# Kernel tuning notes

Hardware: AMD Instinct MI355X
Metric: run time of the kernel (lower is better)

Reference implementation:

```python
import jax, jax.numpy as jnp
import numpy as np

N, E, HID, H, L, EF = 50000, 640000, 128, 8, 3, 16
C = HID // H  # 16, per-head output channels (concat=True)
NEG_SLOPE = 0.2
LN_EPS = 1e-5


def setup_inputs() -> dict:
    key = jax.random.key(0)
    ks = jax.random.split(key, 12)
    s = 0.05
    x = jax.random.normal(ks[0], (N, HID), jnp.float32)
    batch_index = jnp.sort(jax.random.randint(ks[1], (N,), 0, 64, dtype=jnp.int32))
    edge_index = jax.random.randint(ks[2], (2, E), 0, N, dtype=jnp.int32)
    edge_attr = jax.random.normal(ks[3], (E, EF), jnp.float32)
    # edge_transform: Linear(EF, HID)
    Wt = jax.random.normal(ks[4], (EF, HID), jnp.float32) * s
    bt = jnp.zeros((HID,), jnp.float32)
    # per-layer GATv2 params (stacked over L layers)
    Wl = jax.random.normal(ks[5], (L, HID, HID), jnp.float32) * s  # lin_l (source)
    bl = jnp.zeros((L, HID), jnp.float32)
    Wr = jax.random.normal(ks[6], (L, HID, HID), jnp.float32) * s  # lin_r (target)
    br = jnp.zeros((L, HID), jnp.float32)
    We = jax.random.normal(ks[7], (L, HID, HID), jnp.float32) * s  # lin_edge (no bias)
    att = jax.random.normal(ks[8], (L, H, C), jnp.float32) * s
    bias_o = jnp.zeros((L, HID), jnp.float32)
    ln_g = jnp.ones((L, HID), jnp.float32)
    ln_b = jnp.zeros((L, HID), jnp.float32)
    return dict(x=x, batch_index=batch_index, edge_index=edge_index, edge_attr=edge_attr,
                Wt=Wt, bt=bt, Wl=Wl, bl=bl, Wr=Wr, br=br, We=We, att=att,
                bias_o=bias_o, ln_g=ln_g, ln_b=ln_b)


def _layer_norm(x, g, b):
    mu = jnp.mean(x, axis=-1, keepdims=True)
    var = jnp.var(x, axis=-1, keepdims=True)
    return g * (x - mu) * jax.lax.rsqrt(var + LN_EPS) + b


def _gatv2_layer(x, ea, src, dst, Wl, bl, Wr, br, We, att, bias_o):
    # node transforms: lin_l for source features, lin_r for target features
    xl = (x @ Wl + bl).reshape(N, H, C)
    xr = (x @ Wr + br).reshape(N, H, C)
    em = (ea @ We).reshape(E, H, C)
    # per-edge attention logits (GATv2: leaky_relu AFTER the sum, then dot with att)
    m = jax.nn.leaky_relu(xl[src] + xr[dst] + em, NEG_SLOPE)  # [E,H,C]
    logits = jnp.einsum('ehc,hc->eh', m, att)                  # [E,H]
    # segment softmax over incoming edges of each destination node
    lmax = jax.ops.segment_max(logits, dst, num_segments=N)    # [N,H]
    p = jnp.exp(logits - lmax[dst])
    denom = jax.ops.segment_sum(p, dst, num_segments=N)        # [N,H]
    alpha = p / (denom[dst] + 1e-16)
    # weighted scatter-aggregate of source messages
    out = jax.ops.segment_sum(xl[src] * alpha[:, :, None], dst, num_segments=N)  # [N,H,C]
    return out.reshape(N, HID) + bias_o


def reference(x, batch_index, edge_index, edge_attr, Wt, bt, Wl, bl, Wr, br, We, att, bias_o, ln_g, ln_b):
    src, dst = edge_index[0], edge_index[1]
    ea = edge_attr @ Wt + bt  # shared edge_transform, [E,HID]
    for l in range(L):
        out = _gatv2_layer(x, ea, src, dst, Wl[l], bl[l], Wr[l], br[l], We[l], att[l], bias_o[l])
        out = _layer_norm(out, ln_g[l], ln_b[l])
        x = jax.nn.relu(out) + x  # dropout p=0 -> identity; residual
    return x
```

## Files before the change

kernel.cpp:

```cpp
#include <hip/hip_runtime.h>

#define N_NODES 50000
#define N_EDGES 640000
#define HID 128
#define EF 16
#define NLAYERS 3
#define CHUNK 16
#define SCAN_BLOCKS 196

typedef __attribute__((ext_vector_type(8))) short short8;
typedef __attribute__((ext_vector_type(8))) _Float16 half8;
typedef __attribute__((ext_vector_type(4))) float f32x4;
typedef __attribute__((ext_vector_type(2))) float f32x2;

__device__ __forceinline__ unsigned short f2bf(float f) {
  unsigned int u = __float_as_uint(f);
  u = u + 0x7FFFu + ((u >> 16) & 1u);
  return (unsigned short)(u >> 16);
}

__device__ __forceinline__ unsigned short f2h(float f) {
  _Float16 h = (_Float16)f;
  return *(unsigned short*)&h;
}

__device__ __forceinline__ float dpp_hadd8(float v) {
  int x;
  x = __builtin_amdgcn_update_dpp(0, __float_as_int(v), 0xB1, 0xF, 0xF, true);
  v += __int_as_float(x);
  x = __builtin_amdgcn_update_dpp(0, __float_as_int(v), 0x4E, 0xF, 0xF, true);
  v += __int_as_float(x);
  x = __builtin_amdgcn_update_dpp(0, __float_as_int(v), 0x141, 0xF, 0xF, true);
  v += __int_as_float(x);
  return v;
}

__device__ __forceinline__ f32x2 pk_add(f32x2 a, f32x2 b) {
  f32x2 d;
  asm("v_pk_add_f32 %0, %1, %2" : "=v"(d) : "v"(a), "v"(b));
  return d;
}
__device__ __forceinline__ f32x2 pk_mul(f32x2 a, f32x2 b) {
  f32x2 d;
  asm("v_pk_mul_f32 %0, %1, %2" : "=v"(d) : "v"(a), "v"(b));
  return d;
}

__device__ __forceinline__ int pslot(int j) {
  return (((j >> 4) * 8 + (j & 7)) << 1) + ((j >> 3) & 1);
}

__global__ __launch_bounds__(256) void k_setup(const float* __restrict__ Wt,
                                               const float* __restrict__ bt,
                                               const float* __restrict__ We,
                                               const float* __restrict__ Wl,
                                               const float* __restrict__ Wr,
                                               const float* __restrict__ x,
                                               float* __restrict__ ct,
                                               unsigned short* __restrict__ MtB,
                                               unsigned short* __restrict__ WT,
                                               unsigned short* __restrict__ xbf) {
  int b = blockIdx.x, t = threadIdx.x;
  if (b < 26) {
    int id = b * 256 + t;
    const int total = NLAYERS * (EF + 1) * HID;
    if (id >= total) return;
    int l = id / ((EF + 1) * HID);
    int r = id % ((EF + 1) * HID);
    int row = r / HID;
    int j = r % HID;
    const float* Wel = We + l * HID * HID;
    float s = 0.f;
    if (row < EF) {
      const float* wtr = Wt + row * HID;
      for (int i = 0; i < HID; ++i) s += wtr[i] * Wel[i * HID + j];
      int blk = j >> 4, nn = j & 15;
      size_t base = (size_t)(l * 8 + blk) * 64;
      MtB[(base + (size_t)((row >> 3) * 16 + nn)) * 8 + (row & 7)] = f2h(s);
      MtB[(base + (size_t)((2 + (row >> 3)) * 16 + nn)) * 8 + (row & 7)] = 0;
    } else {
      for (int i = 0; i < HID; ++i) s += bt[i] * Wel[i * HID + j];
      ct[l * HID + pslot(j)] = s;
    }
  } else if (b < 410) {
    int id = (b - 26) * 256 + t;
    int k = id & (HID - 1);
    int n = (id >> 7) & (HID - 1);
    int s = (id >> 14) & 1;
    int l = id >> 15;
    const float* W = (s == 0 ? Wl : Wr) + (size_t)l * HID * HID;
    WT[id] = f2bf(W[k * HID + n]);
  } else {
    int id = (b - 410) * 256 + t;
    const float4* p = (const float4*)(x + (size_t)id * 8);
    float4 a = p[0], bb = p[1];
    unsigned short o[8] = {f2bf(a.x), f2bf(a.y), f2bf(a.z), f2bf(a.w),
                           f2bf(bb.x), f2bf(bb.y), f2bf(bb.z), f2bf(bb.w)};
    *(uint4*)(xbf + (size_t)id * 8) = *(uint4*)o;
  }
}

__global__ __launch_bounds__(256) void k_hist(const int* __restrict__ dst, int* __restrict__ counts) {
  int e = blockIdx.x * 256 + threadIdx.x;
  if (e < N_EDGES) atomicAdd(&counts[dst[e]], 1);
}

__global__ __launch_bounds__(256) void k_scan1(const int* __restrict__ counts,
                                               int* __restrict__ rowptr,
                                               int* __restrict__ bsum) {
  __shared__ int sc[256];
  int t = threadIdx.x;
  int i = blockIdx.x * 256 + t;
  int v = (i < N_NODES) ? counts[i] : 0;
  sc[t] = v;
  __syncthreads();
  for (int off = 1; off < 256; off <<= 1) {
    int u = 0;
    if (t >= off) u = sc[t - off];
    __syncthreads();
    sc[t] += u;
    __syncthreads();
  }
  if (i < N_NODES) rowptr[i] = sc[t] - v;
  if (t == 255) bsum[blockIdx.x] = sc[255];
}

__global__ __launch_bounds__(256) void k_scan2(int* __restrict__ bsum) {
  __shared__ int sc[256];
  int t = threadIdx.x;
  int v = (t < SCAN_BLOCKS) ? bsum[t] : 0;
  sc[t] = v;
  __syncthreads();
  for (int off = 1; off < 256; off <<= 1) {
    int u = 0;
    if (t >= off) u = sc[t - off];
    __syncthreads();
    sc[t] += u;
    __syncthreads();
  }
  bsum[t] = sc[t] - v;
}

__global__ __launch_bounds__(256) void k_scan3(int* __restrict__ rowptr, const int* __restrict__ bsum) {
  int t = threadIdx.x;
  int i = blockIdx.x * 256 + t;
  if (i < N_NODES) rowptr[i] += bsum[blockIdx.x];
  if (i == 0) rowptr[N_NODES] = N_EDGES;
}

__global__ __launch_bounds__(256) void k_fill(const int* __restrict__ src,
                                              const int* __restrict__ dst,
                                              const int* __restrict__ rowptr,
                                              int* __restrict__ fill,
                                              int* __restrict__ ssrc,
                                              const float* __restrict__ eattr,
                                              unsigned short* __restrict__ eaA) {
  int e = blockIdx.x * 256 + threadIdx.x;
  if (e >= N_EDGES) return;
  int d = dst[e];
  int pos = atomicAdd(&fill[d], 1);
  int idx = rowptr[d] + pos;
  ssrc[idx] = src[e] << 6;
  const float* pe = eattr + (size_t)e * EF;
  unsigned short* po = eaA + (size_t)idx * 32;
#pragma unroll
  for (int g = 0; g < 2; ++g) {
    unsigned short o[8];
#pragma unroll
    for (int k = 0; k < 8; ++k) o[k] = f2h(pe[g * 8 + k]);
    *(uint4*)(po + g * 8) = *(uint4*)o;
  }
  uint4 z = {0u, 0u, 0u, 0u};
  *(uint4*)(po + 16) = z;
  *(uint4*)(po + 24) = z;
}

__global__ __launch_bounds__(256) void k_gemm_mfma(const unsigned short* __restrict__ xbf,
                                                   const unsigned short* __restrict__ WTl,
                                                   const float* __restrict__ bl,
                                                   const float* __restrict__ br,
                                                   const float* __restrict__ ctl,
                                                   unsigned short* __restrict__ xlb,
                                                   unsigned short* __restrict__ xrb) {
  __shared__ short As[64 * 136];
  __shared__ short Bs[128 * 136];
  int t = threadIdx.x;
  int s = blockIdx.y;
  int row0 = blockIdx.x * 64;

  const uint4* gx = (const uint4*)xbf;
#pragma unroll
  for (int p = 0; p < 4; ++p) {
    int c = t + p * 256;
    int row = c >> 4, col16 = c & 15;
    int grow = row0 + row;
    if (grow >= N_NODES) grow = N_NODES - 1;
    uint4 v = gx[grow * 16 + col16];
    *(uint4*)(&As[row * 136 + col16 * 8]) = v;
  }
  const uint4* gw = (const uint4*)WTl;
#pragma unroll
  for (int p = 0; p < 8; ++p) {
    int c = t + p * 256;
    int row = c >> 4, col16 = c & 15;
    uint4 v = gw[s * 2048 + row * 16 + col16];
    *(uint4*)(&Bs[row * 136 + col16 * 8]) = v;
  }
  __syncthreads();

  int lane = t & 63, w = t >> 6;
  int quad = lane >> 4, lm = lane & 15;
  f32x4 acc[4][2];
#pragma unroll
  for (int mf = 0; mf < 4; ++mf)
#pragma unroll
    for (int nf = 0; nf < 2; ++nf) acc[mf][nf] = (f32x4)(0.f);

#pragma unroll
  for (int ks = 0; ks < 4; ++ks) {
    short8 af[4], bf[2];
#pragma unroll
    for (int mf = 0; mf < 4; ++mf)
      af[mf] = *(short8*)(&As[(mf * 16 + lm) * 136 + ks * 32 + quad * 8]);
#pragma unroll
    for (int nf = 0; nf < 2; ++nf)
      bf[nf] = *(short8*)(&Bs[(w * 32 + nf * 16 + lm) * 136 + ks * 32 + quad * 8]);
#pragma unroll
    for (int mf = 0; mf < 4; ++mf)
#pragma unroll
      for (int nf = 0; nf < 2; ++nf)
        acc[mf][nf] = __builtin_amdgcn_mfma_f32_16x16x32_bf16(af[mf], bf[nf], acc[mf][nf], 0, 0, 0);
  }

  const float* bias = (s == 0) ? bl : br;
  unsigned short* out = (s == 0) ? xlb : xrb;
#pragma unroll
  for (int nf = 0; nf < 2; ++nf) {
    int n = w * 32 + nf * 16 + lm;
    int slot = pslot(n);
    float bv = bias[n] + ((s == 1) ? ctl[slot] : 0.f);
#pragma unroll
    for (int mf = 0; mf < 4; ++mf) {
#pragma unroll
      for (int r = 0; r < 4; ++r) {
        int grow = row0 + mf * 16 + quad * 4 + r;
        if (grow < N_NODES) out[(size_t)grow * HID + slot] = f2bf(acc[mf][nf][r] + bv);
      }
    }
  }
}

__global__ __launch_bounds__(64) void k_fused(const float* __restrict__ xin,
                                              const unsigned int* __restrict__ xlb,
                                              const unsigned int* __restrict__ xrb,
                                              const int* __restrict__ rowptr,
                                              const int* __restrict__ ssrc,
                                              const unsigned short* __restrict__ eaA,
                                              const unsigned int* __restrict__ MtBl,
                                              const float* __restrict__ att,
                                              const float* __restrict__ bias_o,
                                              const float* __restrict__ lng,
                                              const float* __restrict__ lnb,
                                              float* __restrict__ xout,
                                              unsigned short* __restrict__ xbf_out) {
  __shared__ __align__(16) float em_s[CHUNK * 130];
  __shared__ int src_s[CHUNK + 8];
  int n = blockIdx.x;
  int l = threadIdx.x;
  int lm = l & 15, quad = l >> 4;
  int j0 = (l >> 3) * 16 + (l & 7), j1 = j0 + 8;

  uint4 bfr[8];
  const uint4* mb = (const uint4*)MtBl;
#pragma unroll
  for (int b = 0; b < 8; ++b) bfr[b] = mb[b * 64 + l];

  unsigned int ur = xrb[(size_t)n * 64 + l];
  f32x2 base;
  base.x = __uint_as_float(ur << 16);
  base.y = __uint_as_float(ur & 0xFFFF0000u);
  const float LOG2E = 1.44269504088896340736f;
  f32x2 attp = {att[j0] * LOG2E, att[j1] * LOG2E};
  f32x2 c02 = {0.2f, 0.2f};
  int beg = rowptr[n], end = rowptr[n + 1];

  f32x2 acc = {0.f, 0.f};
  float denom = 0.f;

  for (int c0 = beg; c0 < end; c0 += CHUNK) {
    int cnt = min(CHUNK, end - c0);
    if (l < cnt) src_s[l] = ssrc[c0 + l];
    if (l < 8) src_s[cnt + l] = 0;

    half8 af = *(const half8*)(eaA + (size_t)(c0 + lm) * 32 + quad * 8);
    f32x4 cc[8];
#pragma unroll
    for (int b = 0; b < 8; ++b)
      cc[b] = __builtin_amdgcn_mfma_f32_16x16x32_f16(af, *(half8*)&bfr[b], (f32x4)(0.f), 0, 0, 0);
#pragma unroll
    for (int b = 0; b < 8; ++b)
#pragma unroll
      for (int r = 0; r < 4; ++r)
        em_s[(quad * 4 + r) * 130 + ((b * 8 + (lm & 7)) << 1) + (lm >> 3)] = cc[b][r];

    auto edge = [&](int i, unsigned int u) {
      f32x2 xls;
      xls.x = __uint_as_float(u << 16);
      xls.y = __uint_as_float(u & 0xFFFF0000u);
      f32x2 em = *(const f32x2*)(&em_s[i * 130 + 2 * l]);
      f32x2 m = pk_add(pk_add(base, xls), em);
      f32x2 ms = pk_mul(c02, m);
      m.x = fmaxf(m.x, ms.x);
      m.y = fmaxf(m.y, ms.y);
      f32x2 v2 = pk_mul(m, attp);
      float vs = dpp_hadd8(v2.x + v2.y);
      float p = exp2f(vs);
      denom += p;
      acc.x = fmaf(xls.x, p, acc.x);
      acc.y = fmaf(xls.y, p, acc.y);
    };

    unsigned int cur[4];
#pragma unroll
    for (int q = 0; q < 4; ++q) cur[q] = xlb[src_s[q] + l];
    int cnt4 = cnt & ~3;
    for (int i = 0; i < cnt4; i += 4) {
      unsigned int nxt[4];
#pragma unroll
      for (int q = 0; q < 4; ++q) nxt[q] = xlb[src_s[i + 4 + q] + l];
#pragma unroll
      for (int q = 0; q < 4; ++q) edge(i + q, cur[q]);
#pragma unroll
      for (int q = 0; q < 4; ++q) cur[q] = nxt[q];
    }
#pragma unroll
    for (int q = 0; q < 4; ++q)
      if (cnt4 + q < cnt) edge(cnt4 + q, cur[q]);
  }

  f32x2 outp;
  float inv = 1.f / (denom + 1e-16f);
  outp.x = acc.x * inv + bias_o[j0];
  outp.y = acc.y * inv + bias_o[j1];
  float s1 = outp.x + outp.y;
  float s2 = outp.x * outp.x + outp.y * outp.y;
#pragma unroll
  for (int mask = 1; mask <= 32; mask <<= 1) {
    s1 += __shfl_xor(s1, mask);
    s2 += __shfl_xor(s2, mask);
  }
  float mu = s1 * (1.f / 128.f);
  float var = s2 * (1.f / 128.f) - mu * mu;
  float rs = rsqrtf(var + 1e-5f);
  float y0 = lng[j0] * (outp.x - mu) * rs + lnb[j0];
  float y1 = lng[j1] * (outp.y - mu) * rs + lnb[j1];
  float r0 = fmaxf(y0, 0.f) + xin[(size_t)n * HID + j0];
  float r1 = fmaxf(y1, 0.f) + xin[(size_t)n * HID + j1];
  xout[(size_t)n * HID + j0] = r0;
  xout[(size_t)n * HID + j1] = r1;
  xbf_out[(size_t)n * HID + j0] = f2bf(r0);
  xbf_out[(size_t)n * HID + j1] = f2bf(r1);
}

extern "C" void kernel_launch(void* const* d_in, const int* in_sizes, int n_in,
                              void* d_out, int out_size, void* d_ws, size_t ws_size,
                              hipStream_t stream) {
  const float* x0    = (const float*)d_in[0];
  const int*   eidx  = (const int*)d_in[2];
  const float* eattr = (const float*)d_in[3];
  const float* Wt    = (const float*)d_in[4];
  const float* bt    = (const float*)d_in[5];
  const float* Wl    = (const float*)d_in[6];
  const float* bl    = (const float*)d_in[7];
  const float* Wr    = (const float*)d_in[8];
  const float* br    = (const float*)d_in[9];
  const float* We    = (const float*)d_in[10];
  const float* att   = (const float*)d_in[11];
  const float* bo    = (const float*)d_in[12];
  const float* lng   = (const float*)d_in[13];
  const float* lnb   = (const float*)d_in[14];
  float* out = (float*)d_out;
  const int* src = eidx;
  const int* dst = eidx + N_EDGES;

  char* ws = (char*)d_ws;
  size_t off = 0;
  auto alloc = [&](size_t bytes) {
    char* p = ws + off;
    off += (bytes + 255) & ~(size_t)255;
    return p;
  };
  int* counts = (int*)alloc((size_t)N_NODES * 4);
  int* fill   = (int*)alloc((size_t)N_NODES * 4);
  float* ct   = (float*)alloc((size_t)NLAYERS * HID * 4);
  int* rowptr = (int*)alloc((size_t)(N_NODES + 1) * 4);
  int* bsum   = (int*)alloc(256 * 4);
  int* ssrc   = (int*)alloc((size_t)N_EDGES * 4);
  unsigned short* eaA = (unsigned short*)alloc(((size_t)N_EDGES + 16) * 32 * 2);
  unsigned short* MtB = (unsigned short*)alloc((size_t)NLAYERS * 8 * 64 * 8 * 2);
  unsigned short* xlb = (unsigned short*)alloc((size_t)N_NODES * HID * 2);
  unsigned short* xrb = (unsigned short*)alloc((size_t)N_NODES * HID * 2);
  float* xbuf = (float*)alloc((size_t)N_NODES * HID * 4);
  unsigned short* xbf = (unsigned short*)alloc((size_t)N_NODES * HID * 2);
  unsigned short* WTb = (unsigned short*)alloc((size_t)NLAYERS * 2 * HID * HID * 2);

  hipMemsetAsync(counts, 0, (char*)(fill + N_NODES) - (char*)counts, stream);

  hipLaunchKernelGGL(k_setup, dim3(3535), dim3(256), 0, stream,
                     Wt, bt, We, Wl, Wr, x0, ct, MtB, WTb, xbf);
  hipLaunchKernelGGL(k_hist, dim3((N_EDGES + 255) / 256), dim3(256), 0, stream, dst, counts);
  hipLaunchKernelGGL(k_scan1, dim3(SCAN_BLOCKS), dim3(256), 0, stream, counts, rowptr, bsum);
  hipLaunchKernelGGL(k_scan2, dim3(1), dim3(256), 0, stream, bsum);
  hipLaunchKernelGGL(k_scan3, dim3(SCAN_BLOCKS), dim3(256), 0, stream, rowptr, bsum);
  hipLaunchKernelGGL(k_fill, dim3((N_EDGES + 255) / 256), dim3(256), 0, stream,
                     src, dst, rowptr, fill, ssrc, eattr, eaA);

  for (int l = 0; l < NLAYERS; ++l) {
    const float* xin = (l == 0) ? x0 : (const float*)xbuf;
    float* xout = (l == NLAYERS - 1) ? out : xbuf;
    hipLaunchKernelGGL(k_gemm_mfma, dim3((N_NODES + 63) / 64, 2), dim3(256), 0, stream,
                       xbf, WTb + (size_t)l * 2 * HID * HID, bl + l * HID, br + l * HID,
                       ct + (size_t)l * HID, xlb, xrb);
    hipLaunchKernelGGL(k_fused, dim3(N_NODES), dim3(64), 0, stream,
                       xin, (const unsigned int*)xlb, (const unsigned int*)xrb,
                       rowptr, ssrc, eaA,
                       (const unsigned int*)(MtB + (size_t)l * 8 * 64 * 8),
                       att + l * HID,
                       bo + l * HID, lng + l * HID, lnb + l * HID, xout, xbf);
  }
}
```

Before: 441.3 us.

## Merge histogram into setup, store edge terms as fp16 pairs, prefetch 8 sources

Measured after the change: 505.3 us. 14.5% more time.

```diff
diff --git a/kernel.cpp b/kernel.cpp
--- a/kernel.cpp
+++ b/kernel.cpp
@@ -10,6 +10,7 @@
 
 typedef __attribute__((ext_vector_type(8))) short short8;
 typedef __attribute__((ext_vector_type(8))) _Float16 half8;
+typedef __attribute__((ext_vector_type(2))) __fp16 fp16x2;
 typedef __attribute__((ext_vector_type(4))) float f32x4;
 typedef __attribute__((ext_vector_type(2))) float f32x2;
 
@@ -56,6 +57,8 @@
                                                const float* __restrict__ Wl,
                                                const float* __restrict__ Wr,
                                                const float* __restrict__ x,
+                                               const int* __restrict__ dst,
+                                               int* __restrict__ counts,
                                                float* __restrict__ ct,
                                                unsigned short* __restrict__ MtB,
                                                unsigned short* __restrict__ WT,
@@ -90,19 +93,17 @@
     int l = id >> 15;
     const float* W = (s == 0 ? Wl : Wr) + (size_t)l * HID * HID;
     WT[id] = f2bf(W[k * HID + n]);
-  } else {
+  } else if (b < 3535) {
     int id = (b - 410) * 256 + t;
     const float4* p = (const float4*)(x + (size_t)id * 8);
     float4 a = p[0], bb = p[1];
     unsigned short o[8] = {f2bf(a.x), f2bf(a.y), f2bf(a.z), f2bf(a.w),
                            f2bf(bb.x), f2bf(bb.y), f2bf(bb.z), f2bf(bb.w)};
     *(uint4*)(xbf + (size_t)id * 8) = *(uint4*)o;
-  }
-}
-
-__global__ __launch_bounds__(256) void k_hist(const int* __restrict__ dst, int* __restrict__ counts) {
-  int e = blockIdx.x * 256 + threadIdx.x;
-  if (e < N_EDGES) atomicAdd(&counts[dst[e]], 1);
+  } else {
+    int e = (b - 3535) * 256 + t;
+    if (e < N_EDGES) atomicAdd(&counts[dst[e]], 1);
+  }
 }
 
 __global__ __launch_bounds__(256) void k_scan1(const int* __restrict__ counts,
@@ -263,7 +264,7 @@
                                               const float* __restrict__ lnb,
                                               float* __restrict__ xout,
                                               unsigned short* __restrict__ xbf_out) {
-  __shared__ __align__(16) float em_s[CHUNK * 130];
+  __shared__ unsigned int em16_s[CHUNK * 66];
   __shared__ int src_s[CHUNK + 8];
   int n = blockIdx.x;
   int l = threadIdx.x;
@@ -298,16 +299,29 @@
     for (int b = 0; b < 8; ++b)
       cc[b] = __builtin_amdgcn_mfma_f32_16x16x32_f16(af, *(half8*)&bfr[b], (f32x4)(0.f), 0, 0, 0);
 #pragma unroll
-    for (int b = 0; b < 8; ++b)
-#pragma unroll
-      for (int r = 0; r < 4; ++r)
-        em_s[(quad * 4 + r) * 130 + ((b * 8 + (lm & 7)) << 1) + (lm >> 3)] = cc[b][r];
+    for (int b = 0; b < 8; ++b) {
+      unsigned int wv[4];
+#pragma unroll
+      for (int r = 0; r < 4; ++r) {
+        float own = cc[b][r];
+        int pb = __builtin_amdgcn_update_dpp(0, __float_as_int(own), 0x128, 0xF, 0xF, true);
+        fp16x2 pk = __builtin_amdgcn_cvt_pkrtz(own, __int_as_float(pb));
+        wv[r] = *(unsigned int*)&pk;
+      }
+      if (lm < 8) {
+#pragma unroll
+        for (int r = 0; r < 4; ++r)
+          em16_s[(quad * 4 + r) * 66 + b * 8 + lm] = wv[r];
+      }
+    }
 
     auto edge = [&](int i, unsigned int u) {
       f32x2 xls;
       xls.x = __uint_as_float(u << 16);
       xls.y = __uint_as_float(u & 0xFFFF0000u);
-      f32x2 em = *(const f32x2*)(&em_s[i * 130 + 2 * l]);
+      union { unsigned int u32; _Float16 h[2]; } cv;
+      cv.u32 = em16_s[i * 66 + l];
+      f32x2 em = {(float)cv.h[0], (float)cv.h[1]};
       f32x2 m = pk_add(pk_add(base, xls), em);
       f32x2 ms = pk_mul(c02, m);
       m.x = fmaxf(m.x, ms.x);
@@ -320,22 +334,22 @@
       acc.y = fmaf(xls.y, p, acc.y);
     };
 
-    unsigned int cur[4];
-#pragma unroll
-    for (int q = 0; q < 4; ++q) cur[q] = xlb[src_s[q] + l];
-    int cnt4 = cnt & ~3;
-    for (int i = 0; i < cnt4; i += 4) {
-      unsigned int nxt[4];
-#pragma unroll
-      for (int q = 0; q < 4; ++q) nxt[q] = xlb[src_s[i + 4 + q] + l];
-#pragma unroll
-      for (int q = 0; q < 4; ++q) edge(i + q, cur[q]);
-#pragma unroll
-      for (int q = 0; q < 4; ++q) cur[q] = nxt[q];
+    unsigned int cur[8];
+#pragma unroll
+    for (int q = 0; q < 8; ++q) cur[q] = xlb[src_s[q] + l];
+    int cnt8 = cnt & ~7;
+    for (int i = 0; i < cnt8; i += 8) {
+      unsigned int nxt[8];
+#pragma unroll
+      for (int q = 0; q < 8; ++q) nxt[q] = xlb[src_s[i + 8 + q] + l];
+#pragma unroll
+      for (int q = 0; q < 8; ++q) edge(i + q, cur[q]);
+#pragma unroll
+      for (int q = 0; q < 8; ++q) cur[q] = nxt[q];
     }
 #pragma unroll
-    for (int q = 0; q < 4; ++q)
-      if (cnt4 + q < cnt) edge(cnt4 + q, cur[q]);
+    for (int q = 0; q < 8; ++q)
+      if (cnt8 + q < cnt) edge(cnt8 + q, cur[q]);
   }
 
   f32x2 outp;
@@ -406,9 +420,8 @@
 
   hipMemsetAsync(counts, 0, (char*)(fill + N_NODES) - (char*)counts, stream);
 
-  hipLaunchKernelGGL(k_setup, dim3(3535), dim3(256), 0, stream,
-                     Wt, bt, We, Wl, Wr, x0, ct, MtB, WTb, xbf);
-  hipLaunchKernelGGL(k_hist, dim3((N_EDGES + 255) / 256), dim3(256), 0, stream, dst, counts);
+  hipLaunchKernelGGL(k_setup, dim3(6035), dim3(256), 0, stream,
+                     Wt, bt, We, Wl, Wr, x0, dst, counts, ct, MtB, WTb, xbf);
   hipLaunchKernelGGL(k_scan1, dim3(SCAN_BLOCKS), dim3(256), 0, stream, counts, rowptr, bsum);
   hipLaunchKernelGGL(k_scan2, dim3(1), dim3(256), 0, stream, bsum);
   hipLaunchKernelGGL(k_scan3, dim3(SCAN_BLOCKS), dim3(256), 0, stream, rowptr, bsum);
```
